# Kernel optimization log

Hardware: AMD Instinct MI355X
Metric: run time of the kernel (lower is better)

## Reference

```python
import jax, jax.numpy as jnp
import numpy as np

B_SZ, SEQ, D_IN, D_HID, D_OUT = 32, 1024, 128, 256, 128
N_FREQ = SEQ // 2 + 1


def setup_inputs() -> dict:
    key = jax.random.key(0)
    ks = jax.random.split(key, 10)
    s_w = 1.0 / np.sqrt(D_IN)
    return {
        "x": jax.random.normal(ks[0], (B_SZ, SEQ, D_IN), dtype=jnp.float32),
        "W_re": jax.random.uniform(ks[1], (N_FREQ, D_IN, D_HID), minval=-s_w, maxval=s_w, dtype=jnp.float32),
        "W_im": jax.random.uniform(ks[2], (N_FREQ, D_IN, D_HID), minval=-s_w, maxval=s_w, dtype=jnp.float32),
        "B_re": jax.random.uniform(ks[3], (N_FREQ, D_HID), minval=-s_w, maxval=s_w, dtype=jnp.float32),
        "B_im": jax.random.uniform(ks[4], (N_FREQ, D_HID), minval=-s_w, maxval=s_w, dtype=jnp.float32),
        "W_rc": jax.random.uniform(ks[5], (D_IN, D_HID), minval=-s_w, maxval=s_w, dtype=jnp.float32),
        "fc1_w": jax.random.uniform(ks[6], (D_HID, D_HID), minval=-1/np.sqrt(D_HID), maxval=1/np.sqrt(D_HID), dtype=jnp.float32),
        "fc1_b": jnp.zeros((D_HID,), dtype=jnp.float32),
        "fc2_w": jax.random.uniform(ks[7], (D_HID, D_OUT), minval=-1/np.sqrt(D_HID), maxval=1/np.sqrt(D_HID), dtype=jnp.float32),
        "fc2_b": jnp.zeros((D_OUT,), dtype=jnp.float32),
    }


def reference(x, W_re, W_im, B_re, B_im, W_rc, fc1_w, fc1_b, fc2_w, fc2_b):
    # residual channel projection: [b,t,d] @ [d,k] -> [b,t,k]
    x_rc = jnp.einsum("btd,dk->btk", x, W_rc)
    # FFT-domain per-frequency complex MLP
    x_fft = jnp.fft.rfft(x, axis=1)  # [b, n_freq, d] complex
    W = W_re + 1j * W_im             # [n_freq, d, k]
    Bc = B_re + 1j * B_im            # [n_freq, k]
    out = jnp.einsum("bti,tio->bto", x_fft, W) + Bc
    # split-ReLU on real/imag parts, recombine as complex
    out = jax.nn.relu(out.real) + 1j * jax.nn.relu(out.imag)
    out = jnp.fft.irfft(out, n=x.shape[1], axis=1)  # [b, t, k] real
    out = out + x_rc
    # 2-layer MLP head with LeakyReLU (slope 0.01)
    h = jax.nn.leaky_relu(out @ fc1_w + fc1_b, negative_slope=0.01)
    return h @ fc2_w + fc2_b
```

## Files before the change

### kernel.cpp

```cpp
#include <hip/hip_runtime.h>
#include <math.h>

#define NB 32
#define NT 1024
#define ND 128
#define NK 256
#define NO 128
#define NF 513

#define PAD(e) ((e) + ((e) >> 4))

typedef __attribute__((ext_vector_type(8))) short bf16x8;
typedef __attribute__((ext_vector_type(4))) float f32x4;

__device__ __forceinline__ unsigned short f2bf(float f) {
  union { float f; unsigned u; } v; v.f = f;
  return (unsigned short)((v.u + 0x7fffu + ((v.u >> 16) & 1u)) >> 16);
}
__device__ __forceinline__ float bf2f(unsigned u) {
  union { unsigned u; float f; } v; v.u = u << 16;
  return v.f;
}
__device__ __forceinline__ unsigned packbf(float re, float im) {
  return (unsigned)f2bf(re) | ((unsigned)f2bf(im) << 16);
}
__device__ __forceinline__ unsigned digrev4(unsigned j) {
  unsigned r = __brev(j) >> 22;
  return ((r & 0x2AAu) >> 1) | ((r & 0x155u) << 1);
}

template <bool INV>
__device__ void fft1024_r4(float* __restrict__ ar, float* __restrict__ ai,
                           const float* __restrict__ twc,
                           const float* __restrict__ tws, int l) {
  for (int j = l; j < 1024; j += 64) {
    int r = (int)digrev4((unsigned)j);
    if (j < r) {
      int pj = PAD(j), pr = PAD(r);
      float t0 = ar[pj], t1 = ai[pj];
      ar[pj] = ar[pr]; ai[pj] = ai[pr];
      ar[pr] = t0; ai[pr] = t1;
    }
  }
#pragma unroll
  for (int s = 0; s < 5; ++s) {
    const int sh = 2 * s;
    const int q = 1 << sh;
#pragma unroll
    for (int it = 0; it < 4; ++it) {
      int m = it * 64 + l;
      int r = m & (q - 1);
      int i0 = ((m >> sh) << (sh + 2)) + r;
      int p0 = PAD(i0), p1 = PAD(i0 + q), p2 = PAD(i0 + 2 * q), p3 = PAD(i0 + 3 * q);
      float x0r = ar[p0], x0i = ai[p0];
      float x1r = ar[p1], x1i = ai[p1];
      float x2r = ar[p2], x2i = ai[p2];
      float x3r = ar[p3], x3i = ai[p3];
      float t1r, t1i, t2r, t2i, t3r, t3i;
      if (s == 0) {
        t1r = x1r; t1i = x1i; t2r = x2r; t2i = x2i; t3r = x3r; t3i = x3i;
      } else {
        int e = r << (8 - sh);
        float c1 = twc[e], s1 = tws[e];
        float c2 = c1 * c1 - s1 * s1, s2 = 2.0f * c1 * s1;
        float c3 = c1 * c2 - s1 * s2, s3 = c1 * s2 + s1 * c2;
        t1r = x1r * c1 - x1i * s1; t1i = x1r * s1 + x1i * c1;
        t2r = x2r * c2 - x2i * s2; t2i = x2r * s2 + x2i * c2;
        t3r = x3r * c3 - x3i * s3; t3i = x3r * s3 + x3i * c3;
      }
      float u0r = x0r + t2r, u0i = x0i + t2i;
      float u1r = x0r - t2r, u1i = x0i - t2i;
      float u2r = t1r + t3r, u2i = t1i + t3i;
      float u3r = t1r - t3r, u3i = t1i - t3i;
      ar[p0] = u0r + u2r; ai[p0] = u0i + u2i;
      ar[p2] = u0r - u2r; ai[p2] = u0i - u2i;
      if (INV) {
        ar[p1] = u1r - u3i; ai[p1] = u1i + u3r;
        ar[p3] = u1r + u3i; ai[p3] = u1i - u3r;
      } else {
        ar[p1] = u1r + u3i; ai[p1] = u1i - u3r;
        ar[p3] = u1r - u3i; ai[p3] = u1i + u3r;
      }
    }
  }
}

__global__ __launch_bounds__(512, 4) void rfft_kernel(const float* __restrict__ x,
                                                      unsigned* __restrict__ Xc) {
  __shared__ float ar[8 * 1088], ai_[8 * 1088];
  __shared__ float twc[768], tws[768];
  const int tid = threadIdx.x;
  const int b = blockIdx.x >> 3;
  const int c0 = (blockIdx.x & 7) << 4;
  for (int k = tid; k < 768; k += 512) {
    float s, c;
    sincosf(6.283185307179586f * (float)k / 1024.0f, &s, &c);
    twc[k] = c; tws[k] = -s;
  }
  const float* xb = x + (size_t)b * NT * ND + c0;
  for (int idx = tid; idx < 8192; idx += 512) {
    int t = idx >> 3, g = idx & 7;
    float2 v = *(const float2*)(xb + (size_t)t * ND + 2 * g);
    int p = g * 1088 + PAD(t);
    ar[p] = v.x; ai_[p] = v.y;
  }
  __syncthreads();
  const int g = tid >> 6, l = tid & 63;
  fft1024_r4<false>(ar + g * 1088, ai_ + g * 1088, twc, tws, l);
  __syncthreads();
  unsigned* Xb = Xc + (size_t)b * NF * ND + c0;
  for (int idx = tid; idx < NF * 8; idx += 512) {
    int f = idx >> 3, gg = idx & 7;
    int mr = (1024 - f) & 1023;
    int pf = gg * 1088 + PAD(f), pm = gg * 1088 + PAD(mr);
    float x1 = ar[pf], y1 = ai_[pf];
    float xr = ar[pm], yr = ai_[pm];
    unsigned e0 = packbf(0.5f * (x1 + xr), 0.5f * (y1 - yr));
    unsigned e1 = packbf(0.5f * (y1 + yr), 0.5f * (xr - x1));
    *(uint2*)(Xb + (size_t)f * ND + 2 * gg) = make_uint2(e0, e1);
  }
}

#define FPB 9
__global__ __launch_bounds__(512, 2) void freq_mfma_kernel(
    const unsigned* __restrict__ Xc, const float* __restrict__ Wre,
    const float* __restrict__ Wim, const float* __restrict__ Bre,
    const float* __restrict__ Bim, unsigned* __restrict__ Fc) {
  __shared__ unsigned short Wl[2][2][64 * 128];
  const int tid = threadIdx.x;
  const int qg = blockIdx.x & 3;
  const int fg = blockIdx.x >> 2;
  const int n0 = qg << 6;
  const int f0 = fg * FPB;
  const int count = (f0 + FPB <= NF) ? FPB : (NF - f0);

  const int sg = tid >> 4;
  const int scq = tid & 15;
  const int wv = tid >> 6, l = tid & 63;
  const int lr = l & 15, lg = l >> 4;
  const int wvn = wv & 3, mh = wv >> 2;
  const int nl = wvn * 16 + lr;
  const int swn = (nl >> 2) ^ ((nl & 3) << 2);
  const int row = mh * 16 + lr;

  float4 wreg[8];

  auto issueW = [&](int f) {
    const float* wr = Wre + (size_t)f * ND * NK + n0 + scq * 4;
    const float* wi = Wim + (size_t)f * ND * NK + n0 + scq * 4;
#pragma unroll
    for (int r = 0; r < 4; ++r) wreg[r] = *(const float4*)(wr + (size_t)(4 * sg + r) * NK);
#pragma unroll
    for (int r = 0; r < 4; ++r) wreg[4 + r] = *(const float4*)(wi + (size_t)(4 * sg + r) * NK);
  };
  auto stageW = [&](int buf) {
#pragma unroll
    for (int w = 0; w < 2; ++w) {
      unsigned short* wl = Wl[buf][w];
      const float* c0 = (const float*)&wreg[w * 4 + 0];
      const float* c1 = (const float*)&wreg[w * 4 + 1];
      const float* c2 = (const float*)&wreg[w * 4 + 2];
      const float* c3 = (const float*)&wreg[w * 4 + 3];
#pragma unroll
      for (int j = 0; j < 4; ++j) {
        int nn = scq * 4 + j;
        int sw = (nn >> 2) ^ ((nn & 3) << 2);
        int off = nn * 128 + (((sg >> 1) ^ sw) << 3) + ((sg & 1) << 2);
        ushort4 v;
        v.x = f2bf(c0[j]); v.y = f2bf(c1[j]);
        v.z = f2bf(c2[j]); v.w = f2bf(c3[j]);
        *(ushort4*)&wl[off] = v;
      }
    }
  };

  issueW(f0);
  for (int i = 0; i < count; ++i) {
    const int f = f0 + i;
    const int buf = i & 1;
    stageW(buf);
    __syncthreads();

    uint4 xreg[8];
    {
      const unsigned* xb = Xc + ((size_t)row * NF + f) * ND + lg * 8;
#pragma unroll
      for (int ks = 0; ks < 4; ++ks) {
        xreg[2 * ks] = *(const uint4*)(xb + ks * 32);
        xreg[2 * ks + 1] = *(const uint4*)(xb + ks * 32 + 4);
      }
    }
    float br = Bre[(size_t)f * NK + n0 + nl];
    float bi = Bim[(size_t)f * NK + n0 + nl];
    if (i + 1 < count) issueW(f + 1);

    f32x4 aR = (f32x4){br, br, br, br};
    f32x4 aI = (f32x4){bi, bi, bi, bi};
#pragma unroll
    for (int ks = 0; ks < 4; ++ks) {
      int kb = ks * 4 + lg;
      uint4 a0 = xreg[2 * ks], a1 = xreg[2 * ks + 1];
      union { bf16x8 v; unsigned u[4]; } xr, xi, xn;
      xr.u[0] = (a0.x & 0xffffu) | (a0.y << 16);
      xr.u[1] = (a0.z & 0xffffu) | (a0.w << 16);
      xr.u[2] = (a1.x & 0xffffu) | (a1.y << 16);
      xr.u[3] = (a1.z & 0xffffu) | (a1.w << 16);
      xi.u[0] = (a0.x >> 16) | (a0.y & 0xffff0000u);
      xi.u[1] = (a0.z >> 16) | (a0.w & 0xffff0000u);
      xi.u[2] = (a1.x >> 16) | (a1.y & 0xffff0000u);
      xi.u[3] = (a1.z >> 16) | (a1.w & 0xffff0000u);
      xn.u[0] = xi.u[0] ^ 0x80008000u;
      xn.u[1] = xi.u[1] ^ 0x80008000u;
      xn.u[2] = xi.u[2] ^ 0x80008000u;
      xn.u[3] = xi.u[3] ^ 0x80008000u;
      bf16x8 bR = *(const bf16x8*)&Wl[buf][0][nl * 128 + ((kb ^ swn) << 3)];
      bf16x8 bI = *(const bf16x8*)&Wl[buf][1][nl * 128 + ((kb ^ swn) << 3)];
      aR = __builtin_amdgcn_mfma_f32_16x16x32_bf16(xr.v, bR, aR, 0, 0, 0);
      aR = __builtin_amdgcn_mfma_f32_16x16x32_bf16(xn.v, bI, aR, 0, 0, 0);
      aI = __builtin_amdgcn_mfma_f32_16x16x32_bf16(xr.v, bI, aI, 0, 0, 0);
      aI = __builtin_amdgcn_mfma_f32_16x16x32_bf16(xi.v, bR, aI, 0, 0, 0);
    }
#pragma unroll
    for (int r = 0; r < 4; ++r) {
      int brow = mh * 16 + lg * 4 + r;
      float vR = fmaxf(aR[r], 0.0f);
      float vI = fmaxf(aI[r], 0.0f);
      Fc[((size_t)brow * NF + f) * NK + n0 + nl] = packbf(vR, vI);
    }
  }
}

__global__ __launch_bounds__(512, 4) void irfft_kernel(const unsigned* __restrict__ Fc,
                                                       unsigned short* __restrict__ yf) {
  __shared__ float ar[8 * 1088], ai_[8 * 1088];
  __shared__ float twc[768], tws[768];
  const int tid = threadIdx.x;
  const int b = blockIdx.x >> 4;
  const int k0 = (blockIdx.x & 15) << 4;
  for (int k = tid; k < 768; k += 512) {
    float s, c;
    sincosf(6.283185307179586f * (float)k / 1024.0f, &s, &c);
    twc[k] = c; tws[k] = s;
  }
  for (int idx = tid; idx < 8192; idx += 512) {
    int f = idx >> 3, g = idx & 7;
    int src = (f <= 512) ? f : 1024 - f;
    uint2 u = *(const uint2*)(Fc + ((size_t)b * NF + src) * NK + k0 + 2 * g);
    float arr = bf2f(u.x & 0xffff), ari = bf2f(u.x >> 16);
    float brr = bf2f(u.y & 0xffff), bri = bf2f(u.y >> 16);
    float zr, zi;
    if (f <= 512) { zr = arr - bri; zi = ari + brr; }
    else          { zr = arr + bri; zi = brr - ari; }
    int p = g * 1088 + PAD(f);
    ar[p] = zr; ai_[p] = zi;
  }
  __syncthreads();
  const int g = tid >> 6, l = tid & 63;
  fft1024_r4<true>(ar + g * 1088, ai_ + g * 1088, twc, tws, l);
  __syncthreads();
  const float sc = 1.0f / 1024.0f;
  unsigned* yb = (unsigned*)(yf + (size_t)b * NT * NK + k0);
  for (int idx = tid; idx < 8192; idx += 512) {
    int t = idx >> 3, gg = idx & 7;
    int p = gg * 1088 + PAD(t);
    yb[(size_t)t * (NK / 2) + gg] = packbf(ar[p] * sc, ai_[p] * sc);
  }
}

__global__ __launch_bounds__(256) void wconv_kernel(const float* __restrict__ Wrc,
                                                    const float* __restrict__ W1,
                                                    const float* __restrict__ W2,
                                                    unsigned short* __restrict__ Wt) {
  int i = blockIdx.x * 256 + threadIdx.x;
  if (i < 32768) {
    int k = i >> 8, n = i & 255;
    Wt[n * 128 + k] = f2bf(Wrc[i]);
  } else if (i < 98304) {
    int j = i - 32768; int k = j >> 8, n = j & 255;
    Wt[32768 + n * 256 + k] = f2bf(W1[j]);
  } else if (i < 131072) {
    int j = i - 98304; int k = j >> 7, n = j & 127;
    Wt[98304 + n * 256 + k] = f2bf(W2[j]);
  }
}

__global__ __launch_bounds__(512, 4) void mlp_fused_kernel(
    const float* __restrict__ x, const unsigned short* __restrict__ yf,
    const unsigned short* __restrict__ Wt, const float* __restrict__ b1,
    const float* __restrict__ b2, float* __restrict__ out) {
  __shared__ unsigned short y_l[64 * 256];
  __shared__ unsigned short u_l[64 * 256];
  const int tid = threadIdx.x;
  const int wv = tid >> 6, l = tid & 63;
  const int lr = l & 15, lg = l >> 4;
  const int row0 = blockIdx.x * 64;
  const unsigned short* W1_t = Wt + 32768;
  const unsigned short* W2_t = Wt + 98304;

#pragma unroll
  for (int it = 0; it < 4; ++it) {
    int idx = it * 512 + tid;
    int row = idx >> 5, c4 = idx & 31;
    float4 v = *(const float4*)(x + (size_t)(row0 + row) * ND + c4 * 4);
    int blk = (c4 >> 1) ^ (row & 15);
    unsigned short* p = &u_l[row * 128 + blk * 8 + (c4 & 1) * 4];
    p[0] = f2bf(v.x); p[1] = f2bf(v.y); p[2] = f2bf(v.z); p[3] = f2bf(v.w);
  }
  __syncthreads();

  f32x4 acc[4][2];
#pragma unroll
  for (int m = 0; m < 4; ++m)
#pragma unroll
    for (int nt = 0; nt < 2; ++nt) acc[m][nt] = (f32x4){0.f, 0.f, 0.f, 0.f};
#pragma unroll
  for (int ks = 0; ks < 4; ++ks) {
    bf16x8 bb[2];
#pragma unroll
    for (int nt = 0; nt < 2; ++nt) {
      int col = wv * 32 + nt * 16 + lr;
      bb[nt] = *(const bf16x8*)&Wt[col * 128 + ks * 32 + lg * 8];
    }
    bf16x8 aa[4];
#pragma unroll
    for (int m = 0; m < 4; ++m) {
      int row = m * 16 + lr;
      aa[m] = *(const bf16x8*)&u_l[row * 128 + (((ks * 4 + lg) ^ (row & 15)) << 3)];
    }
#pragma unroll
    for (int m = 0; m < 4; ++m)
#pragma unroll
      for (int nt = 0; nt < 2; ++nt)
        acc[m][nt] = __builtin_amdgcn_mfma_f32_16x16x32_bf16(aa[m], bb[nt], acc[m][nt], 0, 0, 0);
  }
#pragma unroll
  for (int m = 0; m < 4; ++m)
#pragma unroll
    for (int nt = 0; nt < 2; ++nt)
#pragma unroll
      for (int r = 0; r < 4; ++r) {
        int row = m * 16 + lg * 4 + r;
        int col = wv * 32 + nt * 16 + lr;
        float v = acc[m][nt][r] + bf2f(yf[(size_t)(row0 + row) * NK + col]);
        int blk = (col >> 3) ^ (row & 31);
        y_l[row * 256 + blk * 8 + (col & 7)] = f2bf(v);
      }
  __syncthreads();

  f32x4 a2[4][2];
  {
    float bv0 = b1[wv * 32 + lr], bv1 = b1[wv * 32 + 16 + lr];
#pragma unroll
    for (int m = 0; m < 4; ++m) {
      a2[m][0] = (f32x4){bv0, bv0, bv0, bv0};
      a2[m][1] = (f32x4){bv1, bv1, bv1, bv1};
    }
  }
#pragma unroll
  for (int ks = 0; ks < 8; ++ks) {
    bf16x8 bb[2];
#pragma unroll
    for (int nt = 0; nt < 2; ++nt) {
      int col = wv * 32 + nt * 16 + lr;
      bb[nt] = *(const bf16x8*)&W1_t[col * 256 + ks * 32 + lg * 8];
    }
    bf16x8 aa[4];
#pragma unroll
    for (int m = 0; m < 4; ++m) {
      int row = m * 16 + lr;
      aa[m] = *(const bf16x8*)&y_l[row * 256 + (((ks * 4 + lg) ^ (row & 31)) << 3)];
    }
#pragma unroll
    for (int m = 0; m < 4; ++m)
#pragma unroll
      for (int nt = 0; nt < 2; ++nt)
        a2[m][nt] = __builtin_amdgcn_mfma_f32_16x16x32_bf16(aa[m], bb[nt], a2[m][nt], 0, 0, 0);
  }
#pragma unroll
  for (int m = 0; m < 4; ++m)
#pragma unroll
    for (int nt = 0; nt < 2; ++nt)
#pragma unroll
      for (int r = 0; r < 4; ++r) {
        int row = m * 16 + lg * 4 + r;
        int col = wv * 32 + nt * 16 + lr;
        float v = a2[m][nt][r];
        v = (v > 0.0f) ? v : 0.01f * v;
        int blk = (col >> 3) ^ (row & 31);
        u_l[row * 256 + blk * 8 + (col & 7)] = f2bf(v);
      }
  __syncthreads();

  const int col3 = wv * 16 + lr;
  f32x4 a3[4];
  {
    float bv = b2[col3];
#pragma unroll
    for (int m = 0; m < 4; ++m) a3[m] = (f32x4){bv, bv, bv, bv};
  }
#pragma unroll
  for (int ks = 0; ks < 8; ++ks) {
    bf16x8 bb = *(const bf16x8*)&W2_t[col3 * 256 + ks * 32 + lg * 8];
    bf16x8 aa[4];
#pragma unroll
    for (int m = 0; m < 4; ++m) {
      int row = m * 16 + lr;
      aa[m] = *(const bf16x8*)&u_l[row * 256 + (((ks * 4 + lg) ^ (row & 31)) << 3)];
    }
#pragma unroll
    for (int m = 0; m < 4; ++m)
      a3[m] = __builtin_amdgcn_mfma_f32_16x16x32_bf16(aa[m], bb, a3[m], 0, 0, 0);
  }
#pragma unroll
  for (int m = 0; m < 4; ++m)
#pragma unroll
    for (int r = 0; r < 4; ++r) {
      int row = m * 16 + lg * 4 + r;
      out[(size_t)(row0 + row) * NO + col3] = a3[m][r];
    }
}

extern "C" void kernel_launch(void* const* d_in, const int* in_sizes, int n_in,
                              void* d_out, int out_size, void* d_ws, size_t ws_size,
                              hipStream_t stream) {
  const float* x     = (const float*)d_in[0];
  const float* W_re  = (const float*)d_in[1];
  const float* W_im  = (const float*)d_in[2];
  const float* B_re  = (const float*)d_in[3];
  const float* B_im  = (const float*)d_in[4];
  const float* W_rc  = (const float*)d_in[5];
  const float* fc1_w = (const float*)d_in[6];
  const float* fc1_b = (const float*)d_in[7];
  const float* fc2_w = (const float*)d_in[8];
  const float* fc2_b = (const float*)d_in[9];
  float* out = (float*)d_out;

  const size_t SZ_X = (size_t)NB * NF * ND;
  const size_t SZ_F = (size_t)NB * NF * NK;
  const size_t SZ_Y = (size_t)NB * NT * NK;
  unsigned* Xc = (unsigned*)d_ws;
  unsigned* Fc = Xc + SZ_X;
  unsigned short* yf = (unsigned short*)(Fc + SZ_F);
  unsigned short* Wt = yf + SZ_Y;

  wconv_kernel<<<dim3(512), dim3(256), 0, stream>>>(W_rc, fc1_w, fc2_w, Wt);
  rfft_kernel<<<dim3(NB * 8), dim3(512), 0, stream>>>(x, Xc);
  freq_mfma_kernel<<<dim3(4 * 57), dim3(512), 0, stream>>>(Xc, W_re, W_im, B_re, B_im, Fc);
  irfft_kernel<<<dim3(NB * 16), dim3(512), 0, stream>>>(Fc, yf);
  mlp_fused_kernel<<<dim3((NB * NT) / 64), dim3(512), 0, stream>>>(x, yf, Wt, fc1_b, fc2_b, out);
}
```

Before: 119.5 us.

## Use one block per frequency with direct global-to-LDS weight loads

The frequency MLP kernel now launches one block per (frequency, 64-column slice) instead of looping over 9 frequencies per block with register double-buffering. Weights are streamed straight into LDS through global_load_lds as fp32, then converted in place to swizzled bf16 tiles, and the launch bounds are raised to allow 4 blocks per CU. The aim is to expose far more parallelism, since the old grid had only 228 blocks, so that the large fp32 weight read (about 268 MB) can saturate HBM bandwidth. In exchange, each block pays extra barriers and a serial load-then-convert phase with no overlap between frequencies.

```diff
diff --git a/kernel.cpp b/kernel.cpp
--- a/kernel.cpp
+++ b/kernel.cpp
@@ -9,6 +9,7 @@
 #define NF 513
 
 #define PAD(e) ((e) + ((e) >> 4))
+#define FSW(n) ((((n) >> 2) & 15) ^ (((n) & 3) << 2))
 
 typedef __attribute__((ext_vector_type(8))) short bf16x8;
 typedef __attribute__((ext_vector_type(4))) float f32x4;
@@ -121,112 +122,132 @@
   }
 }
 
-#define FPB 9
-__global__ __launch_bounds__(512, 2) void freq_mfma_kernel(
+#define WZROW 2064
+#define WZONE 33024
+#define BF_RE 33024
+#define BF_IM 49408
+__global__ __launch_bounds__(512, 4) void freq_mfma_kernel(
     const unsigned* __restrict__ Xc, const float* __restrict__ Wre,
     const float* __restrict__ Wim, const float* __restrict__ Bre,
     const float* __restrict__ Bim, unsigned* __restrict__ Fc) {
-  __shared__ unsigned short Wl[2][2][64 * 128];
+  __shared__ __align__(16) unsigned char raw[66048];
   const int tid = threadIdx.x;
-  const int qg = blockIdx.x & 3;
-  const int fg = blockIdx.x >> 2;
-  const int n0 = qg << 6;
-  const int f0 = fg * FPB;
-  const int count = (f0 + FPB <= NF) ? FPB : (NF - f0);
-
-  const int sg = tid >> 4;
-  const int scq = tid & 15;
+  const int f = blockIdx.x >> 2;
+  const int n0 = (blockIdx.x & 3) << 6;
   const int wv = tid >> 6, l = tid & 63;
+
+  {
+    const float* wb0 = Wre + (size_t)f * ND * NK + n0;
+    const float* wb1 = Wim + (size_t)f * ND * NK + n0;
+#pragma unroll
+    for (int u = 0; u < 8; ++u) {
+      int gu = wv * 8 + u;
+      int which = gu >> 5;
+      int r = gu & 31;
+      int nq = r >> 1, half = r & 1;
+      int k = half * 64 + l;
+      const float* src = (which ? wb1 : wb0) + (size_t)k * NK + nq * 4;
+      void* dst = (void*)(raw + which * WZONE + nq * WZROW + half * 1024);
+      __builtin_amdgcn_global_load_lds(
+          (const __attribute__((address_space(1))) void*)src,
+          (__attribute__((address_space(3))) void*)(unsigned)(size_t)dst,
+          16, 0, 0);
+    }
+  }
+
   const int lr = l & 15, lg = l >> 4;
   const int wvn = wv & 3, mh = wv >> 2;
+  const int row = mh * 16 + lr;
   const int nl = wvn * 16 + lr;
-  const int swn = (nl >> 2) ^ ((nl & 3) << 2);
-  const int row = mh * 16 + lr;
-
-  float4 wreg[8];
-
-  auto issueW = [&](int f) {
-    const float* wr = Wre + (size_t)f * ND * NK + n0 + scq * 4;
-    const float* wi = Wim + (size_t)f * ND * NK + n0 + scq * 4;
-#pragma unroll
-    for (int r = 0; r < 4; ++r) wreg[r] = *(const float4*)(wr + (size_t)(4 * sg + r) * NK);
-#pragma unroll
-    for (int r = 0; r < 4; ++r) wreg[4 + r] = *(const float4*)(wi + (size_t)(4 * sg + r) * NK);
-  };
-  auto stageW = [&](int buf) {
-#pragma unroll
-    for (int w = 0; w < 2; ++w) {
-      unsigned short* wl = Wl[buf][w];
-      const float* c0 = (const float*)&wreg[w * 4 + 0];
-      const float* c1 = (const float*)&wreg[w * 4 + 1];
-      const float* c2 = (const float*)&wreg[w * 4 + 2];
-      const float* c3 = (const float*)&wreg[w * 4 + 3];
-#pragma unroll
-      for (int j = 0; j < 4; ++j) {
-        int nn = scq * 4 + j;
-        int sw = (nn >> 2) ^ ((nn & 3) << 2);
-        int off = nn * 128 + (((sg >> 1) ^ sw) << 3) + ((sg & 1) << 2);
-        ushort4 v;
-        v.x = f2bf(c0[j]); v.y = f2bf(c1[j]);
-        v.z = f2bf(c2[j]); v.w = f2bf(c3[j]);
-        *(ushort4*)&wl[off] = v;
-      }
-    }
-  };
-
-  issueW(f0);
-  for (int i = 0; i < count; ++i) {
-    const int f = f0 + i;
-    const int buf = i & 1;
-    stageW(buf);
+  uint4 xreg[8];
+  {
+    const unsigned* xb = Xc + ((size_t)row * NF + f) * ND + lg * 8;
+#pragma unroll
+    for (int ks = 0; ks < 4; ++ks) {
+      xreg[2 * ks] = *(const uint4*)(xb + ks * 32);
+      xreg[2 * ks + 1] = *(const uint4*)(xb + ks * 32 + 4);
+    }
+  }
+  const float br = Bre[(size_t)f * NK + n0 + nl];
+  const float bi = Bim[(size_t)f * NK + n0 + nl];
+  __syncthreads();
+
+  const int nq = tid & 15, kg = tid >> 4;
+  const int ib = kg >> 1, hf = kg & 1;
+  {
+    float4 q0 = *(const float4*)(raw + WZONE + nq * WZROW + (kg * 4 + 0) * 16);
+    float4 q1 = *(const float4*)(raw + WZONE + nq * WZROW + (kg * 4 + 1) * 16);
+    float4 q2 = *(const float4*)(raw + WZONE + nq * WZROW + (kg * 4 + 2) * 16);
+    float4 q3 = *(const float4*)(raw + WZONE + nq * WZROW + (kg * 4 + 3) * 16);
     __syncthreads();
-
-    uint4 xreg[8];
-    {
-      const unsigned* xb = Xc + ((size_t)row * NF + f) * ND + lg * 8;
-#pragma unroll
-      for (int ks = 0; ks < 4; ++ks) {
-        xreg[2 * ks] = *(const uint4*)(xb + ks * 32);
-        xreg[2 * ks + 1] = *(const uint4*)(xb + ks * 32 + 4);
-      }
-    }
-    float br = Bre[(size_t)f * NK + n0 + nl];
-    float bi = Bim[(size_t)f * NK + n0 + nl];
-    if (i + 1 < count) issueW(f + 1);
-
-    f32x4 aR = (f32x4){br, br, br, br};
-    f32x4 aI = (f32x4){bi, bi, bi, bi};
-#pragma unroll
-    for (int ks = 0; ks < 4; ++ks) {
-      int kb = ks * 4 + lg;
-      uint4 a0 = xreg[2 * ks], a1 = xreg[2 * ks + 1];
-      union { bf16x8 v; unsigned u[4]; } xr, xi, xn;
-      xr.u[0] = (a0.x & 0xffffu) | (a0.y << 16);
-      xr.u[1] = (a0.z & 0xffffu) | (a0.w << 16);
-      xr.u[2] = (a1.x & 0xffffu) | (a1.y << 16);
-      xr.u[3] = (a1.z & 0xffffu) | (a1.w << 16);
-      xi.u[0] = (a0.x >> 16) | (a0.y & 0xffff0000u);
-      xi.u[1] = (a0.z >> 16) | (a0.w & 0xffff0000u);
-      xi.u[2] = (a1.x >> 16) | (a1.y & 0xffff0000u);
-      xi.u[3] = (a1.z >> 16) | (a1.w & 0xffff0000u);
-      xn.u[0] = xi.u[0] ^ 0x80008000u;
-      xn.u[1] = xi.u[1] ^ 0x80008000u;
-      xn.u[2] = xi.u[2] ^ 0x80008000u;
-      xn.u[3] = xi.u[3] ^ 0x80008000u;
-      bf16x8 bR = *(const bf16x8*)&Wl[buf][0][nl * 128 + ((kb ^ swn) << 3)];
-      bf16x8 bI = *(const bf16x8*)&Wl[buf][1][nl * 128 + ((kb ^ swn) << 3)];
-      aR = __builtin_amdgcn_mfma_f32_16x16x32_bf16(xr.v, bR, aR, 0, 0, 0);
-      aR = __builtin_amdgcn_mfma_f32_16x16x32_bf16(xn.v, bI, aR, 0, 0, 0);
-      aI = __builtin_amdgcn_mfma_f32_16x16x32_bf16(xr.v, bI, aI, 0, 0, 0);
-      aI = __builtin_amdgcn_mfma_f32_16x16x32_bf16(xi.v, bR, aI, 0, 0, 0);
-    }
-#pragma unroll
-    for (int r = 0; r < 4; ++r) {
-      int brow = mh * 16 + lg * 4 + r;
-      float vR = fmaxf(aR[r], 0.0f);
-      float vI = fmaxf(aI[r], 0.0f);
-      Fc[((size_t)brow * NF + f) * NK + n0 + nl] = packbf(vR, vI);
-    }
+    unsigned short* bfim = (unsigned short*)(raw + BF_IM);
+    const float* c0 = (const float*)&q0;
+    const float* c1 = (const float*)&q1;
+    const float* c2 = (const float*)&q2;
+    const float* c3 = (const float*)&q3;
+#pragma unroll
+    for (int j = 0; j < 4; ++j) {
+      int n = nq * 4 + j;
+      ushort4 v;
+      v.x = f2bf(c0[j]); v.y = f2bf(c1[j]); v.z = f2bf(c2[j]); v.w = f2bf(c3[j]);
+      *(ushort4*)&bfim[n * 128 + ((ib ^ FSW(n)) << 3) + (hf << 2)] = v;
+    }
+  }
+  {
+    float4 q0 = *(const float4*)(raw + nq * WZROW + (kg * 4 + 0) * 16);
+    float4 q1 = *(const float4*)(raw + nq * WZROW + (kg * 4 + 1) * 16);
+    float4 q2 = *(const float4*)(raw + nq * WZROW + (kg * 4 + 2) * 16);
+    float4 q3 = *(const float4*)(raw + nq * WZROW + (kg * 4 + 3) * 16);
+    unsigned short* bfre = (unsigned short*)(raw + BF_RE);
+    const float* c0 = (const float*)&q0;
+    const float* c1 = (const float*)&q1;
+    const float* c2 = (const float*)&q2;
+    const float* c3 = (const float*)&q3;
+#pragma unroll
+    for (int j = 0; j < 4; ++j) {
+      int n = nq * 4 + j;
+      ushort4 v;
+      v.x = f2bf(c0[j]); v.y = f2bf(c1[j]); v.z = f2bf(c2[j]); v.w = f2bf(c3[j]);
+      *(ushort4*)&bfre[n * 128 + ((ib ^ FSW(n)) << 3) + (hf << 2)] = v;
+    }
+  }
+  __syncthreads();
+
+  const unsigned short* bfre = (const unsigned short*)(raw + BF_RE);
+  const unsigned short* bfim = (const unsigned short*)(raw + BF_IM);
+  const int swn = FSW(nl);
+  f32x4 aR = (f32x4){br, br, br, br};
+  f32x4 aI = (f32x4){bi, bi, bi, bi};
+#pragma unroll
+  for (int ks = 0; ks < 4; ++ks) {
+    int kb = ks * 4 + lg;
+    uint4 a0 = xreg[2 * ks], a1 = xreg[2 * ks + 1];
+    union { bf16x8 v; unsigned u[4]; } xr, xi, xn;
+    xr.u[0] = (a0.x & 0xffffu) | (a0.y << 16);
+    xr.u[1] = (a0.z & 0xffffu) | (a0.w << 16);
+    xr.u[2] = (a1.x & 0xffffu) | (a1.y << 16);
+    xr.u[3] = (a1.z & 0xffffu) | (a1.w << 16);
+    xi.u[0] = (a0.x >> 16) | (a0.y & 0xffff0000u);
+    xi.u[1] = (a0.z >> 16) | (a0.w & 0xffff0000u);
+    xi.u[2] = (a1.x >> 16) | (a1.y & 0xffff0000u);
+    xi.u[3] = (a1.z >> 16) | (a1.w & 0xffff0000u);
+    xn.u[0] = xi.u[0] ^ 0x80008000u;
+    xn.u[1] = xi.u[1] ^ 0x80008000u;
+    xn.u[2] = xi.u[2] ^ 0x80008000u;
+    xn.u[3] = xi.u[3] ^ 0x80008000u;
+    bf16x8 bR = *(const bf16x8*)&bfre[nl * 128 + ((kb ^ swn) << 3)];
+    bf16x8 bI = *(const bf16x8*)&bfim[nl * 128 + ((kb ^ swn) << 3)];
+    aR = __builtin_amdgcn_mfma_f32_16x16x32_bf16(xr.v, bR, aR, 0, 0, 0);
+    aR = __builtin_amdgcn_mfma_f32_16x16x32_bf16(xn.v, bI, aR, 0, 0, 0);
+    aI = __builtin_amdgcn_mfma_f32_16x16x32_bf16(xr.v, bI, aI, 0, 0, 0);
+    aI = __builtin_amdgcn_mfma_f32_16x16x32_bf16(xi.v, bR, aI, 0, 0, 0);
+  }
+#pragma unroll
+  for (int r = 0; r < 4; ++r) {
+    int brow = mh * 16 + lg * 4 + r;
+    float vR = fmaxf(aR[r], 0.0f);
+    float vI = fmaxf(aI[r], 0.0f);
+    Fc[((size_t)brow * NF + f) * NK + n0 + nl] = packbf(vR, vI);
   }
 }
 
@@ -445,7 +466,7 @@
 
   wconv_kernel<<<dim3(512), dim3(256), 0, stream>>>(W_rc, fc1_w, fc2_w, Wt);
   rfft_kernel<<<dim3(NB * 8), dim3(512), 0, stream>>>(x, Xc);
-  freq_mfma_kernel<<<dim3(4 * 57), dim3(512), 0, stream>>>(Xc, W_re, W_im, B_re, B_im, Fc);
+  freq_mfma_kernel<<<dim3(4 * NF), dim3(512), 0, stream>>>(Xc, W_re, W_im, B_re, B_im, Fc);
   irfft_kernel<<<dim3(NB * 16), dim3(512), 0, stream>>>(Fc, yf);
   mlp_fused_kernel<<<dim3((NB * NT) / 64), dim3(512), 0, stream>>>(x, yf, Wt, fc1_b, fc2_b, out);
 }
```

After: 125.7 us. 5.1% more time.
